# Performance work log

Measured on AMD Instinct MI355X. Metric: run time of the kernel, lower is better.

The kernel has to match this reference:

```python
import jax, jax.numpy as jnp
import numpy as np

N, C, D = 4, 1024, 768
H, E, M, P, R = 12, 24, 4, 552, 97
OFFSET = 1  # bert offset for [CLS]


def setup_inputs() -> dict:
    key = jax.random.key(0)
    ks = jax.random.split(key, 16)
    s = 0.02
    return {
        'sequence_output': jax.random.normal(ks[0], (N, C, D), jnp.float32),
        'attention': jax.random.uniform(ks[1], (N, H, C, C), jnp.float32),
        'entity_pos': jax.random.randint(ks[2], (N, E, M), 0, C - 2),
        'hts': jax.random.randint(ks[3], (N, P, 2), 0, E),
        'rels': jax.random.normal(ks[4], (R, D), jnp.float32),
        'We': jax.random.normal(ks[5], (3 * D, D), jnp.float32) * s,
        'be': jnp.zeros((D,), jnp.float32),
        'Wq': jax.random.normal(ks[6], (D, D), jnp.float32) * s,
        'bq': jnp.zeros((D,), jnp.float32),
        'Wk': jax.random.normal(ks[7], (D, D), jnp.float32) * s,
        'bk': jnp.zeros((D,), jnp.float32),
        'Wv': jax.random.normal(ks[8], (D, D), jnp.float32) * s,
        'bv': jnp.zeros((D,), jnp.float32),
        'ln_g': jnp.ones((D,), jnp.float32),
        'ln_b': jnp.zeros((D,), jnp.float32),
        'Wc': jax.random.normal(ks[9], (D, R), jnp.float32) * s,
        'bc': jnp.zeros((R,), jnp.float32),
    }


def reference(sequence_output, attention, entity_pos, hts, rels,
              We, be, Wq, bq, Wk, bk, Wv, bv, ln_g, ln_b, Wc, bc):
    n, c, d = sequence_output.shape
    h = attention.shape[1]
    hd = d // h
    b3 = jnp.arange(n)[:, None, None]
    pos = entity_pos + OFFSET                                  # [n,E,M]
    # --- get_hrt: mention gathers + logsumexp / mean pooling ---
    ment_emb = sequence_output[b3, pos]                        # [n,E,M,d]
    ent_emb = jax.nn.logsumexp(ment_emb, axis=2)               # [n,E,d]
    ment_att = attention[b3, :, pos]                           # [n,E,M,h,c]
    ent_att = ment_att.mean(axis=2)                            # [n,E,h,c]
    hi, ti = hts[..., 0], hts[..., 1]                          # [n,P]
    b2 = jnp.arange(n)[:, None]
    hs = ent_emb[b2, hi]                                       # [n,P,d]
    ts = ent_emb[b2, ti]
    h_att = ent_att[b2, hi]                                    # [n,P,h,c]
    t_att = ent_att[b2, ti]
    ht_att = (h_att * t_att).mean(axis=2)                      # [n,P,c]
    ht_att = ht_att / (ht_att.sum(-1, keepdims=True) + 1e-5)
    rs = jnp.einsum('npc,ncd->npd', ht_att, sequence_output)   # [n,P,d]
    # --- extractor ---
    htr = jnp.tanh(jnp.concatenate([hs, ts, rs], axis=-1) @ We + be)  # [n,P,d]
    # --- double-softmax MultiHeadAttention (eval: dropout = identity) ---
    p = htr.shape[1]
    q = (htr @ Wq + bq).reshape(n, p, h, hd).transpose(2, 0, 1, 3)    # [h,n,P,hd]
    k = (rels @ Wk + bk).reshape(-1, h, hd).transpose(1, 0, 2)        # [h,R,hd]
    v = (rels @ Wv + bv).reshape(-1, h, hd).transpose(1, 0, 2)
    inv_sqrt_d = 1.0 / jnp.sqrt(jnp.float32(d))
    scores = jnp.einsum('hnpe,hre->hnpr', q, k) * inv_sqrt_d
    out = jnp.einsum('hnpr,hre->hnpe', jax.nn.softmax(scores, axis=-1), v)
    scores2 = jnp.einsum('hnpe,hnqe->hnpq', out, out) * inv_sqrt_d
    out = jnp.einsum('hnpq,hnqe->hnpe', jax.nn.softmax(scores2, axis=-1), out)
    out = jnp.tanh(out.transpose(1, 2, 0, 3).reshape(n, p, d))
    # --- residual + LayerNorm + classifier ---
    x = htr + out
    mu = x.mean(-1, keepdims=True)
    var = ((x - mu) ** 2).mean(-1, keepdims=True)
    x = (x - mu) / jnp.sqrt(var + 1e-5) * ln_g + ln_b
    logits = x.reshape(n * p, d) @ Wc + bc                      # [n*P, R]
    return logits
```

## Files before the change

kernel.cpp:

```cpp
#include <hip/hip_runtime.h>
#include <hip/hip_bf16.h>

#define N_ 4
#define C_ 1024
#define D_ 768
#define H_ 12
#define E_ 24
#define M_ 4
#define P_ 552
#define R_ 97
#define HD_ 64
#define D3_ (3*D_)
#define NP_ (N_*P_)

#define SCALE_ 0.036084391824351615f

typedef __attribute__((ext_vector_type(8))) short v8s;
typedef __attribute__((ext_vector_type(4))) float v4f;

__device__ inline ushort f2bf(float x) {
    union { float f; unsigned u; } v; v.f = x;
    unsigned r = (v.u + 0x7FFF + ((v.u >> 16) & 1)) >> 16;
    return (ushort)r;
}

__device__ inline void gl_lds16(const ushort* g, ushort* l) {
    __builtin_amdgcn_global_load_lds(
        (const __attribute__((address_space(1))) unsigned int*)(const void*)g,
        (__attribute__((address_space(3))) unsigned int*)(void*)l,
        16, 0, 0);
}

__device__ inline void tcast32(const float* __restrict__ X, ushort* __restrict__ Xt,
                               int K, int N, int yt, int xt, float (*tile)[33], int t) {
    int row = t >> 5, col = t & 31;
    int r0 = yt * 32, c0 = xt * 32;
    #pragma unroll
    for (int i = 0; i < 4; i++) {
        int r = r0 + row + i*8, c = c0 + col;
        tile[row + i*8][col] = (r < K && c < N) ? X[(long)r*N + c] : 0.f;
    }
    __syncthreads();
    #pragma unroll
    for (int i = 0; i < 4; i++) {
        int n = c0 + row + i*8, k = r0 + col;
        if (n < N && k < K) Xt[(long)n*K + k] = f2bf(tile[col][row + i*8]);
    }
}

__global__ __launch_bounds__(256) void k_prep(
        const float* __restrict__ seq, const float* __restrict__ We,
        const float* __restrict__ Wq, const float* __restrict__ Wk,
        const float* __restrict__ Wv, const float* __restrict__ Wc,
        const float* __restrict__ rels,
        ushort* __restrict__ seqT, ushort* __restrict__ WeT, ushort* __restrict__ W3T,
        ushort* __restrict__ WcT, ushort* __restrict__ relsB) {
    __shared__ float tile[32][33];
    int b = blockIdx.x, t = threadIdx.x;
    if (b < 3072) {
        int z = b / 768, r = b % 768;
        tcast32(seq + (long)z*C_*D_, seqT + (long)z*D_*C_, C_, D_, r/24, r%24, tile, t);
    } else if (b < 4800) {
        int r = b - 3072;
        tcast32(We, WeT, D3_, D_, r/24, r%24, tile, t);
    } else if (b < 6528) {
        int r3 = b - 4800;
        int z = r3 / 576, r = r3 % 576;
        const float* X = (z == 0) ? Wq : (z == 1) ? Wk : Wv;
        tcast32(X, W3T + (size_t)z*D_*D_, D_, D_, r/24, r%24, tile, t);
    } else if (b < 6624) {
        int r = b - 6528;
        tcast32(Wc, WcT, D_, R_, r/4, r%4, tile, t);
    } else {
        int base = (b - 6624) * 1024 + t * 4;
        #pragma unroll
        for (int j = 0; j < 4; j++) {
            int i = base + j;
            if (i < R_*D_) relsB[i] = f2bf(rels[i]);
        }
    }
}

__global__ void k_ent(const float* __restrict__ seq, const float* __restrict__ att,
                      const int* __restrict__ epos,
                      float* __restrict__ entEmb, float* __restrict__ entAtt) {
    int b = blockIdx.x, t = threadIdx.x;
    if (b < 288) {
        int idx = b*256 + t;
        int d  = idx % D_;
        int ne = idx / D_;
        int e  = ne % E_;
        int n  = ne / E_;
        const int* pp = epos + (n*E_ + e)*M_;
        float v[M_];
        float mx = -1e30f;
        #pragma unroll
        for (int m = 0; m < M_; m++) {
            int pos = pp[m] + 1;
            v[m] = seq[((long)n*C_ + pos)*D_ + d];
            mx = fmaxf(mx, v[m]);
        }
        float s = 0.f;
        #pragma unroll
        for (int m = 0; m < M_; m++) s += expf(v[m] - mx);
        entEmb[idx] = mx + logf(s);
    } else {
        long idx = (long)(b - 288)*256 + t;
        int c = idx % C_;
        long r = idx / C_;
        int h = r % H_; r /= H_;
        int e = r % E_;
        int n = r / E_;
        const int* pp = epos + (n*E_ + e)*M_;
        float s = 0.f;
        #pragma unroll
        for (int m = 0; m < M_; m++) {
            int pos = pp[m] + 1;
            s += att[(((long)n*H_ + h)*C_ + pos)*C_ + c];
        }
        entAtt[idx] = s * (1.0f / M_);
    }
}

__global__ void k_gath(const float* __restrict__ entEmb, const float* __restrict__ entAtt,
                       const int* __restrict__ hts,
                       ushort* __restrict__ bcat, ushort* __restrict__ bhtAtt) {
    __shared__ float red[256];
    int b = blockIdx.x, t = threadIdx.x;
    if (b < 6624) {
        int idx = b*256 + t;
        int d  = idx % D_;
        int np = idx / D_;
        int p  = np % P_;
        int n  = np / P_;
        int hi = hts[(n*P_ + p)*2 + 0];
        int ti = hts[(n*P_ + p)*2 + 1];
        bcat[(long)np*D3_ + d]       = f2bf(entEmb[((long)n*E_ + hi)*D_ + d]);
        bcat[(long)np*D3_ + D_ + d]  = f2bf(entEmb[((long)n*E_ + ti)*D_ + d]);
    } else {
        int np = b - 6624;
        int p = np % P_, n = np / P_;
        int hi = hts[(n*P_ + p)*2 + 0];
        int ti = hts[(n*P_ + p)*2 + 1];
        const float* ha = entAtt + ((long)n*E_ + hi)*H_*C_;
        const float* ta = entAtt + ((long)n*E_ + ti)*H_*C_;
        float vals[C_/256];
        float lsum = 0.f;
        #pragma unroll
        for (int i = 0; i < C_/256; i++) {
            int c = t + i*256;
            float s = 0.f;
            #pragma unroll
            for (int h = 0; h < H_; h++) s += ha[h*C_ + c] * ta[h*C_ + c];
            s *= (1.0f / H_);
            vals[i] = s;
            lsum += s;
        }
        red[t] = lsum; __syncthreads();
        for (int s1 = 128; s1; s1 >>= 1) { if (t < s1) red[t] += red[t+s1]; __syncthreads(); }
        float inv = 1.0f / (red[0] + 1e-5f);
        #pragma unroll
        for (int i = 0; i < C_/256; i++)
            bhtAtt[(long)np*C_ + t + i*256] = f2bf(vals[i] * inv);
    }
}

__device__ __forceinline__ void gemm_core(
        int bx, int by,
        const ushort* __restrict__ A, const ushort* __restrict__ Bt,
        const float* __restrict__ bias, float* __restrict__ Cf, ushort* __restrict__ Cb,
        long cfo, long cbo,
        int M, int N, int Npad, int K,
        int lda, int ldb, int ldcf, int ldcb,
        int act, int biasM,
        ushort* __restrict__ As, ushort* __restrict__ Bs) {
    int t = threadIdx.x;
    int m0 = by * 128, n0 = bx * 128;
    int lr = t >> 2;
    int lc = (t & 3) * 8;
    int wv = t >> 6, lane = t & 63;
    int quad = lane >> 4, lm = lane & 15;
    int wm = (wv >> 1) * 64, wn = (wv & 1) * 64;

    const ushort* pA0 = A + (long)min(m0 + lr,      M-1)*lda + lc;
    const ushort* pA1 = A + (long)min(m0 + lr + 64, M-1)*lda + lc;
    const ushort* pB0 = Bt + (long)min(n0 + lr,      N-1)*ldb + lc;
    const ushort* pB1 = Bt + (long)min(n0 + lr + 64, N-1)*ldb + lc;

    v4f acc[4][4];
    #pragma unroll
    for (int i = 0; i < 4; i++)
        #pragma unroll
        for (int j = 0; j < 4; j++)
            acc[i][j] = (v4f){0.f, 0.f, 0.f, 0.f};

    int nIter = K >> 5;
    gl_lds16(pA0, As + t*8);
    gl_lds16(pA1, As + 2048 + t*8);
    gl_lds16(pB0, Bs + t*8);
    gl_lds16(pB1, Bs + 2048 + t*8);
    if (nIter > 1) {
        gl_lds16(pA0 + 32, As + 4096 + t*8);
        gl_lds16(pA1 + 32, As + 4096 + 2048 + t*8);
        gl_lds16(pB0 + 32, Bs + 4096 + t*8);
        gl_lds16(pB1 + 32, Bs + 4096 + 2048 + t*8);
    }

    for (int it = 0; it < nIter; ++it) {
        int cur = (it & 3) * 4096;
        if (it + 2 < nIter) {
            asm volatile("s_waitcnt vmcnt(4)\n\ts_barrier" ::: "memory");
            int nb = ((it + 2) & 3) * 4096;
            int k2 = (it + 2) << 5;
            gl_lds16(pA0 + k2, As + nb + t*8);
            gl_lds16(pA1 + k2, As + nb + 2048 + t*8);
            gl_lds16(pB0 + k2, Bs + nb + t*8);
            gl_lds16(pB1 + k2, Bs + nb + 2048 + t*8);
        } else {
            asm volatile("s_waitcnt vmcnt(0)\n\ts_barrier" ::: "memory");
        }
        v8s a[4], b[4];
        #pragma unroll
        for (int i = 0; i < 4; i++)
            a[i] = *(const v8s*)(As + cur + (wm + i*16 + lm)*32 + quad*8);
        #pragma unroll
        for (int j = 0; j < 4; j++)
            b[j] = *(const v8s*)(Bs + cur + (wn + j*16 + lm)*32 + quad*8);
        #pragma unroll
        for (int i = 0; i < 4; i++)
            #pragma unroll
            for (int j = 0; j < 4; j++)
                acc[i][j] = __builtin_amdgcn_mfma_f32_16x16x32_bf16(a[i], b[j], acc[i][j], 0, 0, 0);
    }

    #pragma unroll
    for (int j = 0; j < 4; j++) {
        int gn = n0 + wn + j*16 + lm;
        if (gn >= Npad) continue;
        bool vld = gn < N;
        float bvn = (bias && !biasM && vld) ? bias[gn] : 0.f;
        #pragma unroll
        for (int i = 0; i < 4; i++) {
            #pragma unroll
            for (int reg = 0; reg < 4; reg++) {
                int gm = m0 + wm + i*16 + quad*4 + reg;
                if (gm >= M) continue;
                float v = 0.f;
                if (vld) {
                    v = acc[i][j][reg] + bvn;
                    if (bias && biasM) v += bias[gm];
                    if (act == 1) v = tanhf(v);
                }
                if (Cf) Cf[cfo + (long)gm*ldcf + gn] = v;
                if (Cb) Cb[cbo + (long)gm*ldcb + gn] = f2bf(v);
            }
        }
    }
}

__global__ __launch_bounds__(256) void k_mfma_bt(
        const ushort* __restrict__ A, const ushort* __restrict__ Bt,
        const float* __restrict__ bias, float* __restrict__ Cf, ushort* __restrict__ Cb,
        int M, int N, int Npad, int K,
        int lda, int ldb, int ldcf, int ldcb, int nb2,
        long sA1, long sA2, long sB1, long sB2,
        long sCf1, long sCf2, long sCb1, long sCb2,
        int act, int biasM) {
    __shared__ ushort As[4][128*32];
    __shared__ ushort Bs[4][128*32];
    int z = blockIdx.z;
    int b1 = z / nb2, b2 = z % nb2;
    gemm_core(blockIdx.x, blockIdx.y,
              A + b1*sA1 + b2*sA2, Bt + b1*sB1 + b2*sB2, bias, Cf, Cb,
              b1*sCf1 + b2*sCf2, b1*sCb1 + b2*sCb2,
              M, N, Npad, K, lda, ldb, ldcf, ldcb, act, biasM,
              &As[0][0], &Bs[0][0]);
}

__global__ __launch_bounds__(256) void k_qkv(
        const ushort* __restrict__ bhtr, const ushort* __restrict__ WqT,
        const ushort* __restrict__ WkT, const ushort* __restrict__ WvT,
        const ushort* __restrict__ relsB,
        const float* __restrict__ bq, const float* __restrict__ bk,
        const float* __restrict__ bv,
        ushort* __restrict__ bqb, ushort* __restrict__ bkb, ushort* __restrict__ vT) {
    __shared__ ushort As[4][128*32];
    __shared__ ushort Bs[4][128*32];
    int x = blockIdx.x, y = blockIdx.y;
    if (y < 18) {
        gemm_core(x, y, bhtr, WqT, bq, nullptr, bqb, 0, 0,
                  NP_, D_, D_, D_, D_, D_, 0, D_, 0, 0, &As[0][0], &Bs[0][0]);
    } else if (y == 18) {
        gemm_core(x, 0, relsB, WkT, bk, nullptr, bkb, 0, 0,
                  R_, D_, D_, D_, D_, D_, 0, D_, 0, 0, &As[0][0], &Bs[0][0]);
    } else if (x == 0) {
        gemm_core(0, y - 19, WvT, relsB, bv, nullptr, vT, 0, 0,
                  D_, R_, 128, D_, D_, D_, 0, 128, 0, 1, &As[0][0], &Bs[0][0]);
    }
}

__global__ __launch_bounds__(256) void k_attn1f(
        const ushort* __restrict__ qb, const ushort* __restrict__ kb,
        const ushort* __restrict__ vT, ushort* __restrict__ o1b) {
    int mt = blockIdx.x, h = blockIdx.y;
    int m0 = mt * 128;
    __shared__ ushort U[128*128];
    __shared__ ushort Vs[64*128];
    __shared__ float rowm[2][128];
    __shared__ float rowl[2][128];
    ushort* Qs = U;
    ushort* Ks = U + 128*64;
    ushort* Ps = U;
    int t = threadIdx.x;
    const uint4 z4 = {0u,0u,0u,0u};
    #pragma unroll
    for (int i = 0; i < 4; i++) {
        int id = t + i*256;
        int row = id >> 3, c8 = (id & 7) * 8;
        int np = m0 + row;
        uint4 qv = z4;
        if (np < NP_) qv = *(const uint4*)(qb + (long)np*D_ + h*HD_ + c8);
        *(uint4*)(Qs + row*64 + c8) = qv;
        uint4 kv = z4;
        if (row < R_) kv = *(const uint4*)(kb + (long)row*D_ + h*HD_ + c8);
        *(uint4*)(Ks + row*64 + c8) = kv;
    }
    #pragma unroll
    for (int i = 0; i < 4; i++) {
        int id = t + i*256;
        int e = id >> 4, c8 = (id & 15) * 8;
        *(uint4*)(Vs + e*128 + c8) = *(const uint4*)(vT + ((long)h*HD_ + e)*128 + c8);
    }
    __syncthreads();
    int wv = t >> 6, lane = t & 63;
    int quad = lane >> 4, lm = lane & 15;
    int wm = (wv >> 1) * 64, wn = (wv & 1) * 64;
    int side = wv & 1;

    v4f acc[4][4];
    #pragma unroll
    for (int i = 0; i < 4; i++)
        #pragma unroll
        for (int j = 0; j < 4; j++)
            acc[i][j] = (v4f){0.f,0.f,0.f,0.f};
    #pragma unroll
    for (int k0 = 0; k0 < 64; k0 += 32) {
        v8s a[4], b[4];
        #pragma unroll
        for (int i = 0; i < 4; i++) a[i] = *(const v8s*)(Qs + (wm + i*16 + lm)*64 + k0 + quad*8);
        #pragma unroll
        for (int j = 0; j < 4; j++) b[j] = *(const v8s*)(Ks + (wn + j*16 + lm)*64 + k0 + quad*8);
        #pragma unroll
        for (int i = 0; i < 4; i++)
            #pragma unroll
            for (int j = 0; j < 4; j++)
                acc[i][j] = __builtin_amdgcn_mfma_f32_16x16x32_bf16(a[i], b[j], acc[i][j], 0, 0, 0);
    }
    #pragma unroll
    for (int j = 0; j < 4; j++) {
        int col = wn + j*16 + lm;
        bool ok = col < R_;
        #pragma unroll
        for (int i = 0; i < 4; i++)
            #pragma unroll
            for (int reg = 0; reg < 4; reg++)
                acc[i][j][reg] = ok ? acc[i][j][reg]*SCALE_ : -1e30f;
    }
    #pragma unroll
    for (int i = 0; i < 4; i++)
        #pragma unroll
        for (int reg = 0; reg < 4; reg++) {
            float m = fmaxf(fmaxf(acc[i][0][reg], acc[i][1][reg]),
                            fmaxf(acc[i][2][reg], acc[i][3][reg]));
            #pragma unroll
            for (int o = 1; o < 16; o <<= 1) m = fmaxf(m, __shfl_xor(m, o));
            if (lm == 0) rowm[side][wm + i*16 + quad*4 + reg] = m;
        }
    __syncthreads();
    #pragma unroll
    for (int i = 0; i < 4; i++)
        #pragma unroll
        for (int reg = 0; reg < 4; reg++) {
            int r = wm + i*16 + quad*4 + reg;
            float m = fmaxf(rowm[0][r], rowm[1][r]);
            float s = 0.f;
            #pragma unroll
            for (int j = 0; j < 4; j++) {
                float e = expf(acc[i][j][reg] - m);
                acc[i][j][reg] = e;
                s += e;
            }
            #pragma unroll
            for (int o = 1; o < 16; o <<= 1) s += __shfl_xor(s, o);
            if (lm == 0) rowl[side][r] = s;
        }
    __syncthreads();
    #pragma unroll
    for (int i = 0; i < 4; i++)
        #pragma unroll
        for (int reg = 0; reg < 4; reg++) {
            int r = wm + i*16 + quad*4 + reg;
            float inv = 1.0f / (rowl[0][r] + rowl[1][r]);
            #pragma unroll
            for (int j = 0; j < 4; j++)
                Ps[r*128 + wn + j*16 + lm] = f2bf(acc[i][j][reg] * inv);
        }
    __syncthreads();
    v4f acc2[2][4];
    #pragma unroll
    for (int i = 0; i < 2; i++)
        #pragma unroll
        for (int j = 0; j < 4; j++)
            acc2[i][j] = (v4f){0.f,0.f,0.f,0.f};
    int wm2 = wv * 32;
    #pragma unroll
    for (int k0 = 0; k0 < 128; k0 += 32) {
        v8s a2[2], b2[4];
        #pragma unroll
        for (int i = 0; i < 2; i++) a2[i] = *(const v8s*)(Ps + (wm2 + i*16 + lm)*128 + k0 + quad*8);
        #pragma unroll
        for (int j = 0; j < 4; j++) b2[j] = *(const v8s*)(Vs + (j*16 + lm)*128 + k0 + quad*8);
        #pragma unroll
        for (int i = 0; i < 2; i++)
            #pragma unroll
            for (int j = 0; j < 4; j++)
                acc2[i][j] = __builtin_amdgcn_mfma_f32_16x16x32_bf16(a2[i], b2[j], acc2[i][j], 0, 0, 0);
    }
    #pragma unroll
    for (int i = 0; i < 2; i++)
        #pragma unroll
        for (int j = 0; j < 4; j++)
            #pragma unroll
            for (int reg = 0; reg < 4; reg++) {
                int row = m0 + wm2 + i*16 + quad*4 + reg;
                if (row >= NP_) continue;
                o1b[(long)row*D_ + h*HD_ + j*16 + lm] = f2bf(acc2[i][j][reg]);
            }
}

__global__ __launch_bounds__(256) void k_attn2f(
        const ushort* __restrict__ o1b, float* __restrict__ o2) {
    int qt = blockIdx.x;
    int zz = blockIdx.y;
    int n = zz / H_, h = zz % H_;
    int q0 = qt * 128;
    __shared__ ushort Qs[128*64];
    __shared__ ushort KV[128*64];
    __shared__ ushort Ps[128*128];
    __shared__ float rowm[2][128], rowl[2][128];
    __shared__ float mrun[128], lrun[128], alphaS[128];
    int t = threadIdx.x;
    const ushort* base = o1b + (long)n*P_*D_ + h*HD_;
    const uint4 z4 = {0u,0u,0u,0u};
    #pragma unroll
    for (int i = 0; i < 4; i++) {
        int id = t + i*256;
        int row = id >> 3, c8 = (id & 7) * 8;
        int q = q0 + row;
        uint4 v = z4;
        if (q < P_) v = *(const uint4*)(base + (long)q*D_ + c8);
        *(uint4*)(Qs + row*64 + c8) = v;
    }
    if (t < 128) { mrun[t] = -1e30f; lrun[t] = 0.f; }
    __syncthreads();
    int wv = t >> 6, lane = t & 63;
    int quad = lane >> 4, lm = lane & 15;
    int wm = (wv >> 1) * 64, wn = (wv & 1) * 64;
    int side = wv & 1;
    int wm2 = wv * 32;
    v4f acc2[2][4];
    #pragma unroll
    for (int i = 0; i < 2; i++)
        #pragma unroll
        for (int j = 0; j < 4; j++)
            acc2[i][j] = (v4f){0.f,0.f,0.f,0.f};

    for (int c = 0; c < 5; c++) {
        #pragma unroll
        for (int i = 0; i < 4; i++) {
            int id = t + i*256;
            int row = id >> 3, c8 = (id & 7) * 8;
            int q = c*128 + row;
            uint4 v = z4;
            if (q < P_) v = *(const uint4*)(base + (long)q*D_ + c8);
            *(uint4*)(KV + row*64 + c8) = v;
        }
        __syncthreads();
        v4f acc[4][4];
        #pragma unroll
        for (int i = 0; i < 4; i++)
            #pragma unroll
            for (int j = 0; j < 4; j++)
                acc[i][j] = (v4f){0.f,0.f,0.f,0.f};
        #pragma unroll
        for (int k0 = 0; k0 < 64; k0 += 32) {
            v8s a[4], b[4];
            #pragma unroll
            for (int i = 0; i < 4; i++) a[i] = *(const v8s*)(Qs + (wm + i*16 + lm)*64 + k0 + quad*8);
            #pragma unroll
            for (int j = 0; j < 4; j++) b[j] = *(const v8s*)(KV + (wn + j*16 + lm)*64 + k0 + quad*8);
            #pragma unroll
            for (int i = 0; i < 4; i++)
                #pragma unroll
                for (int j = 0; j < 4; j++)
                    acc[i][j] = __builtin_amdgcn_mfma_f32_16x16x32_bf16(a[i], b[j], acc[i][j], 0, 0, 0);
        }
        #pragma unroll
        for (int j = 0; j < 4; j++) {
            int col = c*128 + wn + j*16 + lm;
            bool ok = col < P_;
            #pragma unroll
            for (int i = 0; i < 4; i++)
                #pragma unroll
                for (int reg = 0; reg < 4; reg++)
                    acc[i][j][reg] = ok ? acc[i][j][reg]*SCALE_ : -1e30f;
        }
        #pragma unroll
        for (int i = 0; i < 4; i++)
            #pragma unroll
            for (int reg = 0; reg < 4; reg++) {
                float m = fmaxf(fmaxf(acc[i][0][reg], acc[i][1][reg]),
                                fmaxf(acc[i][2][reg], acc[i][3][reg]));
                #pragma unroll
                for (int o = 1; o < 16; o <<= 1) m = fmaxf(m, __shfl_xor(m, o));
                if (lm == 0) rowm[side][wm + i*16 + quad*4 + reg] = m;
            }
        __syncthreads();
        #pragma unroll
        for (int i = 0; i < 4; i++)
            #pragma unroll
            for (int reg = 0; reg < 4; reg++) {
                int r = wm + i*16 + quad*4 + reg;
                float mc = fmaxf(rowm[0][r], rowm[1][r]);
                float mn = fmaxf(mrun[r], mc);
                float s = 0.f;
                #pragma unroll
                for (int j = 0; j < 4; j++) {
                    float e = expf(acc[i][j][reg] - mn);
                    acc[i][j][reg] = e;
                    s += e;
                }
                #pragma unroll
                for (int o = 1; o < 16; o <<= 1) s += __shfl_xor(s, o);
                if (lm == 0) rowl[side][r] = s;
            }
        __syncthreads();
        if (t < 128) {
            float mo = mrun[t];
            float mc = fmaxf(rowm[0][t], rowm[1][t]);
            float mn = fmaxf(mo, mc);
            float al = expf(mo - mn);
            lrun[t] = lrun[t]*al + rowl[0][t] + rowl[1][t];
            mrun[t] = mn;
            alphaS[t] = al;
        }
        #pragma unroll
        for (int i = 0; i < 4; i++) {
            int id = t + i*256;
            int q = id & 127, e0 = (id >> 7) * 8;
            int gq = c*128 + q;
            uint4 v = z4;
            if (gq < P_) v = *(const uint4*)(base + (long)gq*D_ + e0);
            const ushort* pv = (const ushort*)&v;
            #pragma unroll
            for (int j = 0; j < 8; j++) KV[(e0+j)*128 + q] = pv[j];
        }
        #pragma unroll
        for (int i = 0; i < 4; i++)
            #pragma unroll
            for (int reg = 0; reg < 4; reg++) {
                int r = wm + i*16 + quad*4 + reg;
                #pragma unroll
                for (int j = 0; j < 4; j++)
                    Ps[r*128 + wn + j*16 + lm] = f2bf(acc[i][j][reg]);
            }
        __syncthreads();
        #pragma unroll
        for (int i = 0; i < 2; i++) {
            #pragma unroll
            for (int reg = 0; reg < 4; reg++) {
                float al = alphaS[wm2 + i*16 + quad*4 + reg];
                #pragma unroll
                for (int j = 0; j < 4; j++)
                    acc2[i][j][reg] *= al;
            }
        }
        #pragma unroll
        for (int k0 = 0; k0 < 128; k0 += 32) {
            v8s a2[2], b2[4];
            #pragma unroll
            for (int i = 0; i < 2; i++) a2[i] = *(const v8s*)(Ps + (wm2 + i*16 + lm)*128 + k0 + quad*8);
            #pragma unroll
            for (int j = 0; j < 4; j++) b2[j] = *(const v8s*)(KV + (j*16 + lm)*128 + k0 + quad*8);
            #pragma unroll
            for (int i = 0; i < 2; i++)
                #pragma unroll
                for (int j = 0; j < 4; j++)
                    acc2[i][j] = __builtin_amdgcn_mfma_f32_16x16x32_bf16(a2[i], b2[j], acc2[i][j], 0, 0, 0);
        }
        __syncthreads();
    }
    #pragma unroll
    for (int i = 0; i < 2; i++)
        #pragma unroll
        for (int j = 0; j < 4; j++)
            #pragma unroll
            for (int reg = 0; reg < 4; reg++) {
                int row = wm2 + i*16 + quad*4 + reg;
                int q = q0 + row;
                if (q >= P_) continue;
                float l = lrun[row];
                o2[((long)n*P_ + q)*D_ + h*HD_ + j*16 + lm] = acc2[i][j][reg] / l;
            }
}

__global__ void k_ln(const float* __restrict__ htr, const float* __restrict__ o2,
                     const float* __restrict__ g, const float* __restrict__ b,
                     ushort* __restrict__ bx) {
    int np = blockIdx.x;
    int t = threadIdx.x;
    __shared__ float red[256];
    float v[D_/256];
    float s = 0.f;
    #pragma unroll
    for (int i = 0; i < D_/256; i++) {
        int d = t + i*256;
        float val = htr[(long)np*D_ + d] + tanhf(o2[(long)np*D_ + d]);
        v[i] = val; s += val;
    }
    red[t] = s; __syncthreads();
    for (int s1 = 128; s1; s1 >>= 1) { if (t < s1) red[t] += red[t+s1]; __syncthreads(); }
    float mu = red[0] * (1.0f/D_);
    __syncthreads();
    float s2 = 0.f;
    #pragma unroll
    for (int i = 0; i < D_/256; i++) { float dx = v[i]-mu; s2 += dx*dx; }
    red[t] = s2; __syncthreads();
    for (int s1 = 128; s1; s1 >>= 1) { if (t < s1) red[t] += red[t+s1]; __syncthreads(); }
    float inv = rsqrtf(red[0]*(1.0f/D_) + 1e-5f);
    #pragma unroll
    for (int i = 0; i < D_/256; i++) {
        int d = t + i*256;
        bx[(long)np*D_ + d] = f2bf((v[i]-mu)*inv*g[d] + b[d]);
    }
}

extern "C" void kernel_launch(void* const* d_in, const int* in_sizes, int n_in,
                              void* d_out, int out_size, void* d_ws, size_t ws_size,
                              hipStream_t stream) {
    const float* seq   = (const float*)d_in[0];
    const float* att   = (const float*)d_in[1];
    const int*   epos  = (const int*)d_in[2];
    const int*   hts   = (const int*)d_in[3];
    const float* rels  = (const float*)d_in[4];
    const float* We    = (const float*)d_in[5];
    const float* be    = (const float*)d_in[6];
    const float* Wq    = (const float*)d_in[7];
    const float* bq    = (const float*)d_in[8];
    const float* Wk    = (const float*)d_in[9];
    const float* bk    = (const float*)d_in[10];
    const float* Wv    = (const float*)d_in[11];
    const float* bv    = (const float*)d_in[12];
    const float* ln_g  = (const float*)d_in[13];
    const float* ln_b  = (const float*)d_in[14];
    const float* Wc    = (const float*)d_in[15];
    const float* bc    = (const float*)d_in[16];
    float* out = (float*)d_out;
    float* w = (float*)d_ws;

    const int NP = NP_;

    float* entEmb  = w;
    float* entAtt  = entEmb  + (size_t)N_*E_*D_;
    float* htr     = entAtt  + (size_t)N_*E_*H_*C_;
    float* o2      = htr     + (size_t)NP*D_;
    ushort* bhtAtt = (ushort*)(o2 + (size_t)NP*D_);
    ushort* bcat   = bhtAtt + (size_t)NP*C_;
    ushort* seqT   = bcat  + (size_t)NP*D3_;
    ushort* WeT    = seqT  + (size_t)N_*D_*C_;
    ushort* WqT    = WeT   + (size_t)D_*D3_;
    ushort* WkT    = WqT   + (size_t)D_*D_;
    ushort* WvT    = WkT   + (size_t)D_*D_;
    ushort* WcT    = WvT   + (size_t)D_*D_;
    ushort* relsB  = WcT   + (size_t)D_*R_;
    ushort* bhtr   = relsB + (size_t)R_*D_;
    ushort* bqb    = bhtr  + (size_t)NP*D_;
    ushort* bkb    = bqb   + (size_t)NP*D_;
    ushort* vT     = bkb   + (size_t)R_*D_;
    ushort* o1b    = vT    + (size_t)D_*128;
    ushort* bxb    = o1b   + (size_t)NP*D_;

    k_prep<<<6697, 256, 0, stream>>>(seq, We, Wq, Wk, Wv, Wc, rels,
                                     seqT, WeT, WqT, WcT, relsB);
    k_ent<<<4896, 256, 0, stream>>>(seq, att, epos, entEmb, entAtt);
    k_gath<<<8832, 256, 0, stream>>>(entEmb, entAtt, hts, bcat, bhtAtt);

    k_mfma_bt<<<dim3(6, 5, N_), 256, 0, stream>>>(
        bhtAtt, seqT, nullptr, nullptr, bcat + 2*D_,
        P_, D_, D_, C_, C_, C_, 0, D3_, 1,
        (long)P_*C_, 0, (long)D_*C_, 0, 0, 0, (long)P_*D3_, 0, 0, 0);

    k_mfma_bt<<<dim3(6, 18, 1), 256, 0, stream>>>(
        bcat, WeT, be, htr, bhtr,
        NP, D_, D_, D3_, D3_, D3_, D_, D_, 1,
        0, 0, 0, 0, 0, 0, 0, 0, 1, 0);

    k_qkv<<<dim3(6, 25, 1), 256, 0, stream>>>(
        bhtr, WqT, WkT, WvT, relsB, bq, bk, bv, bqb, bkb, vT);

    k_attn1f<<<dim3(18, 12), 256, 0, stream>>>(bqb, bkb, vT, o1b);

    k_attn2f<<<dim3(5, 48), 256, 0, stream>>>(o1b, o2);

    k_ln<<<NP, 256, 0, stream>>>(htr, o2, ln_g, ln_b, bxb);

    k_mfma_bt<<<dim3(1, 18, 1), 256, 0, stream>>>(
        bxb, WcT, bc, out, nullptr,
        NP, R_, R_, D_, D_, D_, R_, 0, 1,
        0, 0, 0, 0, 0, 0, 0, 0, 0, 0);
}
```

Before: 544.3 us.

## Fuse pipeline stages into a persistent megakernel with grid-wide barriers

Merges the prep and entity-pooling kernels into one launch, and runs the gather, the GEMMs, both attention stages, LayerNorm and the classifier inside a single persistent 256-block kernel. Stages are separated by an atomic-counter grid barrier, and stage shared memory is overlaid through a union. The goal is to remove per-launch overhead and the tail gaps between the eight dependent launches. In exchange, every stage is limited to 256 blocks at one block per CU, the gather and LayerNorm stages become strided loops, and the spin barrier relies on all blocks being co-resident.

```diff
diff --git a/kernel.cpp b/kernel.cpp
--- a/kernel.cpp
+++ b/kernel.cpp
@@ -48,85 +48,111 @@
     }
 }
 
-__global__ __launch_bounds__(256) void k_prep(
-        const float* __restrict__ seq, const float* __restrict__ We,
-        const float* __restrict__ Wq, const float* __restrict__ Wk,
-        const float* __restrict__ Wv, const float* __restrict__ Wc,
-        const float* __restrict__ rels,
+__global__ __launch_bounds__(256) void k_prep_ent(
+        const float* __restrict__ seq, const float* __restrict__ att,
+        const int* __restrict__ epos,
+        const float* __restrict__ We, const float* __restrict__ Wq,
+        const float* __restrict__ Wk, const float* __restrict__ Wv,
+        const float* __restrict__ Wc, const float* __restrict__ rels,
         ushort* __restrict__ seqT, ushort* __restrict__ WeT, ushort* __restrict__ W3T,
-        ushort* __restrict__ WcT, ushort* __restrict__ relsB) {
+        ushort* __restrict__ WcT, ushort* __restrict__ relsB,
+        float* __restrict__ entEmb, float* __restrict__ entAtt,
+        int* __restrict__ bar) {
     __shared__ float tile[32][33];
     int b = blockIdx.x, t = threadIdx.x;
-    if (b < 3072) {
-        int z = b / 768, r = b % 768;
-        tcast32(seq + (long)z*C_*D_, seqT + (long)z*D_*C_, C_, D_, r/24, r%24, tile, t);
-    } else if (b < 4800) {
-        int r = b - 3072;
-        tcast32(We, WeT, D3_, D_, r/24, r%24, tile, t);
-    } else if (b < 6528) {
-        int r3 = b - 4800;
-        int z = r3 / 576, r = r3 % 576;
-        const float* X = (z == 0) ? Wq : (z == 1) ? Wk : Wv;
-        tcast32(X, W3T + (size_t)z*D_*D_, D_, D_, r/24, r%24, tile, t);
-    } else if (b < 6624) {
-        int r = b - 6528;
-        tcast32(Wc, WcT, D_, R_, r/4, r%4, tile, t);
+    if (b == 0 && t == 0) *bar = 0;
+    if (b < 6697) {
+        if (b < 3072) {
+            int z = b / 768, r = b % 768;
+            tcast32(seq + (long)z*C_*D_, seqT + (long)z*D_*C_, C_, D_, r/24, r%24, tile, t);
+        } else if (b < 4800) {
+            int r = b - 3072;
+            tcast32(We, WeT, D3_, D_, r/24, r%24, tile, t);
+        } else if (b < 6528) {
+            int r3 = b - 4800;
+            int z = r3 / 576, r = r3 % 576;
+            const float* X = (z == 0) ? Wq : (z == 1) ? Wk : Wv;
+            tcast32(X, W3T + (size_t)z*D_*D_, D_, D_, r/24, r%24, tile, t);
+        } else if (b < 6624) {
+            int r = b - 6528;
+            tcast32(Wc, WcT, D_, R_, r/4, r%4, tile, t);
+        } else {
+            int base = (b - 6624) * 1024 + t * 4;
+            #pragma unroll
+            for (int j = 0; j < 4; j++) {
+                int i = base + j;
+                if (i < R_*D_) relsB[i] = f2bf(rels[i]);
+            }
+        }
     } else {
-        int base = (b - 6624) * 1024 + t * 4;
-        #pragma unroll
-        for (int j = 0; j < 4; j++) {
-            int i = base + j;
-            if (i < R_*D_) relsB[i] = f2bf(rels[i]);
-        }
-    }
-}
-
-__global__ void k_ent(const float* __restrict__ seq, const float* __restrict__ att,
-                      const int* __restrict__ epos,
-                      float* __restrict__ entEmb, float* __restrict__ entAtt) {
-    int b = blockIdx.x, t = threadIdx.x;
-    if (b < 288) {
-        int idx = b*256 + t;
-        int d  = idx % D_;
-        int ne = idx / D_;
-        int e  = ne % E_;
-        int n  = ne / E_;
-        const int* pp = epos + (n*E_ + e)*M_;
-        float v[M_];
-        float mx = -1e30f;
-        #pragma unroll
-        for (int m = 0; m < M_; m++) {
-            int pos = pp[m] + 1;
-            v[m] = seq[((long)n*C_ + pos)*D_ + d];
-            mx = fmaxf(mx, v[m]);
-        }
-        float s = 0.f;
-        #pragma unroll
-        for (int m = 0; m < M_; m++) s += expf(v[m] - mx);
-        entEmb[idx] = mx + logf(s);
-    } else {
-        long idx = (long)(b - 288)*256 + t;
-        int c = idx % C_;
-        long r = idx / C_;
-        int h = r % H_; r /= H_;
-        int e = r % E_;
-        int n = r / E_;
-        const int* pp = epos + (n*E_ + e)*M_;
-        float s = 0.f;
-        #pragma unroll
-        for (int m = 0; m < M_; m++) {
-            int pos = pp[m] + 1;
-            s += att[(((long)n*H_ + h)*C_ + pos)*C_ + c];
-        }
-        entAtt[idx] = s * (1.0f / M_);
-    }
-}
-
-__global__ void k_gath(const float* __restrict__ entEmb, const float* __restrict__ entAtt,
-                       const int* __restrict__ hts,
-                       ushort* __restrict__ bcat, ushort* __restrict__ bhtAtt) {
-    __shared__ float red[256];
-    int b = blockIdx.x, t = threadIdx.x;
+        int b2 = b - 6697;
+        if (b2 < 288) {
+            int idx = b2*256 + t;
+            int d  = idx % D_;
+            int ne = idx / D_;
+            int e  = ne % E_;
+            int n  = ne / E_;
+            const int* pp = epos + (n*E_ + e)*M_;
+            float v[M_];
+            float mx = -1e30f;
+            #pragma unroll
+            for (int m = 0; m < M_; m++) {
+                int pos = pp[m] + 1;
+                v[m] = seq[((long)n*C_ + pos)*D_ + d];
+                mx = fmaxf(mx, v[m]);
+            }
+            float s = 0.f;
+            #pragma unroll
+            for (int m = 0; m < M_; m++) s += expf(v[m] - mx);
+            entEmb[idx] = mx + logf(s);
+        } else {
+            long idx = (long)(b2 - 288)*256 + t;
+            int c = idx % C_;
+            long r = idx / C_;
+            int h = r % H_; r /= H_;
+            int e = r % E_;
+            int n = r / E_;
+            const int* pp = epos + (n*E_ + e)*M_;
+            float s = 0.f;
+            #pragma unroll
+            for (int m = 0; m < M_; m++) {
+                int pos = pp[m] + 1;
+                s += att[(((long)n*H_ + h)*C_ + pos)*C_ + c];
+            }
+            entAtt[idx] = s * (1.0f / M_);
+        }
+    }
+}
+
+union __align__(16) SM {
+    struct { ushort As[4*4096]; ushort Bs[4*4096]; } g;
+    struct { ushort U[128*128]; ushort Vs[64*128];
+             float rowm[2][128]; float rowl[2][128]; } a1;
+    struct { ushort Qs[128*64]; ushort KV[128*64]; ushort Ps[128*128];
+             float rowm[2][128]; float rowl[2][128];
+             float mrun[128]; float lrun[128]; float alphaS[128]; } a2;
+    struct { float red[256]; } r;
+};
+
+__device__ __forceinline__ void gbar(int* bar, int it) {
+    __threadfence();
+    __syncthreads();
+    if (threadIdx.x == 0) {
+        __hip_atomic_fetch_add(bar, 1, __ATOMIC_ACQ_REL, __HIP_MEMORY_SCOPE_AGENT);
+        while (__hip_atomic_load(bar, __ATOMIC_ACQUIRE, __HIP_MEMORY_SCOPE_AGENT) < 256*it) {
+            __builtin_amdgcn_s_sleep(2);
+        }
+    }
+    __syncthreads();
+    __threadfence();
+}
+
+
+__device__ __forceinline__ void gath_one(int b,
+        const float* __restrict__ entEmb, const float* __restrict__ entAtt,
+        const int* __restrict__ hts,
+        ushort* __restrict__ bcat, ushort* __restrict__ bhtAtt, float* red) {
+    int t = threadIdx.x;
     if (b < 6624) {
         int idx = b*256 + t;
         int d  = idx % D_;
@@ -258,59 +284,16 @@
     }
 }
 
-__global__ __launch_bounds__(256) void k_mfma_bt(
-        const ushort* __restrict__ A, const ushort* __restrict__ Bt,
-        const float* __restrict__ bias, float* __restrict__ Cf, ushort* __restrict__ Cb,
-        int M, int N, int Npad, int K,
-        int lda, int ldb, int ldcf, int ldcb, int nb2,
-        long sA1, long sA2, long sB1, long sB2,
-        long sCf1, long sCf2, long sCb1, long sCb2,
-        int act, int biasM) {
-    __shared__ ushort As[4][128*32];
-    __shared__ ushort Bs[4][128*32];
-    int z = blockIdx.z;
-    int b1 = z / nb2, b2 = z % nb2;
-    gemm_core(blockIdx.x, blockIdx.y,
-              A + b1*sA1 + b2*sA2, Bt + b1*sB1 + b2*sB2, bias, Cf, Cb,
-              b1*sCf1 + b2*sCf2, b1*sCb1 + b2*sCb2,
-              M, N, Npad, K, lda, ldb, ldcf, ldcb, act, biasM,
-              &As[0][0], &Bs[0][0]);
-}
-
-__global__ __launch_bounds__(256) void k_qkv(
-        const ushort* __restrict__ bhtr, const ushort* __restrict__ WqT,
-        const ushort* __restrict__ WkT, const ushort* __restrict__ WvT,
-        const ushort* __restrict__ relsB,
-        const float* __restrict__ bq, const float* __restrict__ bk,
-        const float* __restrict__ bv,
-        ushort* __restrict__ bqb, ushort* __restrict__ bkb, ushort* __restrict__ vT) {
-    __shared__ ushort As[4][128*32];
-    __shared__ ushort Bs[4][128*32];
-    int x = blockIdx.x, y = blockIdx.y;
-    if (y < 18) {
-        gemm_core(x, y, bhtr, WqT, bq, nullptr, bqb, 0, 0,
-                  NP_, D_, D_, D_, D_, D_, 0, D_, 0, 0, &As[0][0], &Bs[0][0]);
-    } else if (y == 18) {
-        gemm_core(x, 0, relsB, WkT, bk, nullptr, bkb, 0, 0,
-                  R_, D_, D_, D_, D_, D_, 0, D_, 0, 0, &As[0][0], &Bs[0][0]);
-    } else if (x == 0) {
-        gemm_core(0, y - 19, WvT, relsB, bv, nullptr, vT, 0, 0,
-                  D_, R_, 128, D_, D_, D_, 0, 128, 0, 1, &As[0][0], &Bs[0][0]);
-    }
-}
-
-__global__ __launch_bounds__(256) void k_attn1f(
+__device__ __forceinline__ void attn1_one(int mt, int h,
         const ushort* __restrict__ qb, const ushort* __restrict__ kb,
-        const ushort* __restrict__ vT, ushort* __restrict__ o1b) {
-    int mt = blockIdx.x, h = blockIdx.y;
+        const ushort* __restrict__ vT, ushort* __restrict__ o1b, SM& sm) {
     int m0 = mt * 128;
-    __shared__ ushort U[128*128];
-    __shared__ ushort Vs[64*128];
-    __shared__ float rowm[2][128];
-    __shared__ float rowl[2][128];
-    ushort* Qs = U;
-    ushort* Ks = U + 128*64;
-    ushort* Ps = U;
+    ushort* Qs = sm.a1.U;
+    ushort* Ks = sm.a1.U + 128*64;
+    ushort* Ps = sm.a1.U;
+    ushort* Vs = sm.a1.Vs;
+    auto& rowm = sm.a1.rowm;
+    auto& rowl = sm.a1.rowl;
     int t = threadIdx.x;
     const uint4 z4 = {0u,0u,0u,0u};
     #pragma unroll
@@ -438,17 +421,18 @@
             }
 }
 
-__global__ __launch_bounds__(256) void k_attn2f(
-        const ushort* __restrict__ o1b, float* __restrict__ o2) {
-    int qt = blockIdx.x;
-    int zz = blockIdx.y;
+__device__ __forceinline__ void attn2_one(int qt, int zz,
+        const ushort* __restrict__ o1b, float* __restrict__ o2, SM& sm) {
     int n = zz / H_, h = zz % H_;
     int q0 = qt * 128;
-    __shared__ ushort Qs[128*64];
-    __shared__ ushort KV[128*64];
-    __shared__ ushort Ps[128*128];
-    __shared__ float rowm[2][128], rowl[2][128];
-    __shared__ float mrun[128], lrun[128], alphaS[128];
+    ushort* Qs = sm.a2.Qs;
+    ushort* KV = sm.a2.KV;
+    ushort* Ps = sm.a2.Ps;
+    auto& rowm = sm.a2.rowm;
+    auto& rowl = sm.a2.rowl;
+    float* mrun = sm.a2.mrun;
+    float* lrun = sm.a2.lrun;
+    float* alphaS = sm.a2.alphaS;
     int t = threadIdx.x;
     const ushort* base = o1b + (long)n*P_*D_ + h*HD_;
     const uint4 z4 = {0u,0u,0u,0u};
@@ -614,12 +598,11 @@
             }
 }
 
-__global__ void k_ln(const float* __restrict__ htr, const float* __restrict__ o2,
-                     const float* __restrict__ g, const float* __restrict__ b,
-                     ushort* __restrict__ bx) {
-    int np = blockIdx.x;
+__device__ __forceinline__ void ln_one(int np,
+        const float* __restrict__ htr, const float* __restrict__ o2,
+        const float* __restrict__ g, const float* __restrict__ b,
+        ushort* __restrict__ bx, float* red) {
     int t = threadIdx.x;
-    __shared__ float red[256];
     float v[D_/256];
     float s = 0.f;
     #pragma unroll
@@ -643,6 +626,73 @@
         int d = t + i*256;
         bx[(long)np*D_ + d] = f2bf((v[i]-mu)*inv*g[d] + b[d]);
     }
+}
+
+struct Args {
+    const float *be, *bq, *bk, *bv, *ln_g, *ln_b, *bc;
+    const int *hts;
+    float *out;
+    float *entEmb, *entAtt, *htr, *o2;
+    ushort *bhtAtt, *bcat, *seqT, *WeT, *WqT, *WkT, *WvT, *WcT, *relsB;
+    ushort *bhtr, *bqb, *bkb, *vT, *o1b, *bxb;
+    int *bar;
+};
+
+__global__ __launch_bounds__(256, 1) void k_mega(Args A) {
+    __shared__ SM sm;
+    int bid = blockIdx.x;
+
+    for (int vb = bid; vb < 8832; vb += 256) {
+        gath_one(vb, A.entEmb, A.entAtt, A.hts, A.bcat, A.bhtAtt, sm.r.red);
+        __syncthreads();
+    }
+    gbar(A.bar, 1);
+
+    if (bid < 120) {
+        int x = bid % 6, r = bid / 6, y = r % 5, z = r / 5;
+        gemm_core(x, y, A.bhtAtt + (long)z*P_*C_, A.seqT + (long)z*D_*C_,
+                  nullptr, nullptr, A.bcat + 2*D_,
+                  0, (long)z*P_*D3_,
+                  P_, D_, D_, C_, C_, C_, 0, D3_, 0, 0, sm.g.As, sm.g.Bs);
+    }
+    gbar(A.bar, 2);
+
+    if (bid < 108) {
+        int x = bid % 6, y = bid / 6;
+        gemm_core(x, y, A.bcat, A.WeT, A.be, A.htr, A.bhtr, 0, 0,
+                  NP_, D_, D_, D3_, D3_, D3_, D_, D_, 1, 0, sm.g.As, sm.g.Bs);
+    }
+    gbar(A.bar, 3);
+
+    if (bid < 150) {
+        int x = bid % 6, y = bid / 6;
+        if (y < 18)
+            gemm_core(x, y, A.bhtr, A.WqT, A.bq, nullptr, A.bqb, 0, 0,
+                      NP_, D_, D_, D_, D_, D_, 0, D_, 0, 0, sm.g.As, sm.g.Bs);
+        else if (y == 18)
+            gemm_core(x, 0, A.relsB, A.WkT, A.bk, nullptr, A.bkb, 0, 0,
+                      R_, D_, D_, D_, D_, D_, 0, D_, 0, 0, sm.g.As, sm.g.Bs);
+        else if (x == 0)
+            gemm_core(0, y - 19, A.WvT, A.relsB, A.bv, nullptr, A.vT, 0, 0,
+                      D_, R_, 128, D_, D_, D_, 0, 128, 0, 1, sm.g.As, sm.g.Bs);
+    }
+    gbar(A.bar, 4);
+
+    if (bid < 216) attn1_one(bid % 18, bid / 18, A.bqb, A.bkb, A.vT, A.o1b, sm);
+    gbar(A.bar, 5);
+
+    if (bid < 240) attn2_one(bid % 5, bid / 5, A.o1b, A.o2, sm);
+    gbar(A.bar, 6);
+
+    for (int np = bid; np < NP_; np += 256) {
+        ln_one(np, A.htr, A.o2, A.ln_g, A.ln_b, A.bxb, sm.r.red);
+        __syncthreads();
+    }
+    gbar(A.bar, 7);
+
+    if (bid < 18)
+        gemm_core(0, bid, A.bxb, A.WcT, A.bc, A.out, nullptr, 0, 0,
+                  NP_, R_, R_, D_, D_, D_, R_, 0, 0, 0, sm.g.As, sm.g.Bs);
 }
 
 extern "C" void kernel_launch(void* const* d_in, const int* in_sizes, int n_in,
@@ -668,15 +718,13 @@
     float* out = (float*)d_out;
     float* w = (float*)d_ws;
 
-    const int NP = NP_;
-
     float* entEmb  = w;
     float* entAtt  = entEmb  + (size_t)N_*E_*D_;
     float* htr     = entAtt  + (size_t)N_*E_*H_*C_;
-    float* o2      = htr     + (size_t)NP*D_;
-    ushort* bhtAtt = (ushort*)(o2 + (size_t)NP*D_);
-    ushort* bcat   = bhtAtt + (size_t)NP*C_;
-    ushort* seqT   = bcat  + (size_t)NP*D3_;
+    float* o2      = htr     + (size_t)NP_*D_;
+    ushort* bhtAtt = (ushort*)(o2 + (size_t)NP_*D_);
+    ushort* bcat   = bhtAtt + (size_t)NP_*C_;
+    ushort* seqT   = bcat  + (size_t)NP_*D3_;
     ushort* WeT    = seqT  + (size_t)N_*D_*C_;
     ushort* WqT    = WeT   + (size_t)D_*D3_;
     ushort* WkT    = WqT   + (size_t)D_*D_;
@@ -684,38 +732,25 @@
     ushort* WcT    = WvT   + (size_t)D_*D_;
     ushort* relsB  = WcT   + (size_t)D_*R_;
     ushort* bhtr   = relsB + (size_t)R_*D_;
-    ushort* bqb    = bhtr  + (size_t)NP*D_;
-    ushort* bkb    = bqb   + (size_t)NP*D_;
+    ushort* bqb    = bhtr  + (size_t)NP_*D_;
+    ushort* bkb    = bqb   + (size_t)NP_*D_;
     ushort* vT     = bkb   + (size_t)R_*D_;
     ushort* o1b    = vT    + (size_t)D_*128;
-    ushort* bxb    = o1b   + (size_t)NP*D_;
-
-    k_prep<<<6697, 256, 0, stream>>>(seq, We, Wq, Wk, Wv, Wc, rels,
-                                     seqT, WeT, WqT, WcT, relsB);
-    k_ent<<<4896, 256, 0, stream>>>(seq, att, epos, entEmb, entAtt);
-    k_gath<<<8832, 256, 0, stream>>>(entEmb, entAtt, hts, bcat, bhtAtt);
-
-    k_mfma_bt<<<dim3(6, 5, N_), 256, 0, stream>>>(
-        bhtAtt, seqT, nullptr, nullptr, bcat + 2*D_,
-        P_, D_, D_, C_, C_, C_, 0, D3_, 1,
-        (long)P_*C_, 0, (long)D_*C_, 0, 0, 0, (long)P_*D3_, 0, 0, 0);
-
-    k_mfma_bt<<<dim3(6, 18, 1), 256, 0, stream>>>(
-        bcat, WeT, be, htr, bhtr,
-        NP, D_, D_, D3_, D3_, D3_, D_, D_, 1,
-        0, 0, 0, 0, 0, 0, 0, 0, 1, 0);
-
-    k_qkv<<<dim3(6, 25, 1), 256, 0, stream>>>(
-        bhtr, WqT, WkT, WvT, relsB, bq, bk, bv, bqb, bkb, vT);
-
-    k_attn1f<<<dim3(18, 12), 256, 0, stream>>>(bqb, bkb, vT, o1b);
-
-    k_attn2f<<<dim3(5, 48), 256, 0, stream>>>(o1b, o2);
-
-    k_ln<<<NP, 256, 0, stream>>>(htr, o2, ln_g, ln_b, bxb);
-
-    k_mfma_bt<<<dim3(1, 18, 1), 256, 0, stream>>>(
-        bxb, WcT, bc, out, nullptr,
-        NP, R_, R_, D_, D_, D_, R_, 0, 1,
-        0, 0, 0, 0, 0, 0, 0, 0, 0, 0);
-}
+    ushort* bxb    = o1b   + (size_t)NP_*D_;
+    int*    bar    = (int*)(bxb + (size_t)NP_*D_);
+
+    k_prep_ent<<<11593, 256, 0, stream>>>(seq, att, epos, We, Wq, Wk, Wv, Wc, rels,
+                                          seqT, WeT, WqT, WcT, relsB,
+                                          entEmb, entAtt, bar);
+
+    Args Aa;
+    Aa.be = be; Aa.bq = bq; Aa.bk = bk; Aa.bv = bv;
+    Aa.ln_g = ln_g; Aa.ln_b = ln_b; Aa.bc = bc;
+    Aa.hts = hts; Aa.out = out;
+    Aa.entEmb = entEmb; Aa.entAtt = entAtt; Aa.htr = htr; Aa.o2 = o2;
+    Aa.bhtAtt = bhtAtt; Aa.bcat = bcat; Aa.seqT = seqT; Aa.WeT = WeT;
+    Aa.WqT = WqT; Aa.WkT = WkT; Aa.WvT = WvT; Aa.WcT = WcT; Aa.relsB = relsB;
+    Aa.bhtr = bhtr; Aa.bqb = bqb; Aa.bkb = bkb; Aa.vT = vT; Aa.o1b = o1b; Aa.bxb = bxb;
+    Aa.bar = bar;
+    k_mega<<<256, 256, 0, stream>>>(Aa);
+}
```

Result: slower. 1.249 ms (+129.4%).
